# Performance work log

Hardware: AMD Instinct MI355X
Metric: run time of the kernel (lower is better)

The kernel has to match this reference:

```python
import jax, jax.numpy as jnp
import numpy as np

B, K, D, DS = 32, 64, 4, 4
H = 512            # hidden_dim
HH = H // 2        # hidden_hidden_dim = 256
NA = 2             # n_action


def _lin(k, out_d, in_d):
    kw, kb = jax.random.split(k)
    w = jax.random.normal(kw, (out_d, in_d), dtype=jnp.float32) * (in_d ** -0.5)
    b = jax.random.normal(kb, (out_d,), dtype=jnp.float32) * 0.01
    return w, b


def setup_inputs() -> dict:
    key = jax.random.key(0)
    ks = jax.random.split(key, 16)
    state = jax.random.normal(ks[0], (B, DS), dtype=jnp.float32)
    obs = jax.random.normal(ks[1], (B, D, K), dtype=jnp.float32)
    layer_w, layer_b = _lin(ks[2], H, DS)
    e1_w, e1_b = _lin(ks[3], H, 2 * D)
    e2_w, e2_b = _lin(ks[4], H, H)
    e3_w, e3_b = _lin(ks[5], H, H)
    ln_g = jnp.ones((H,), jnp.float32)
    ln_b = jnp.zeros((H,), jnp.float32)
    n1_w, n1_b = _lin(ks[6], H, D + H + DS)
    n2_w, n2_b = _lin(ks[7], HH, H)
    mu1_w, mu1_b = _lin(ks[8], 256, H + H)
    mu2_w, mu2_b = _lin(ks[9], 128, 256)
    mu3_w, mu3_b = _lin(ks[10], NA, 128)
    s1_w, s1_b = _lin(ks[11], 256, H + H)
    s2_w, s2_b = _lin(ks[12], 128, 256)
    s3_w, s3_b = _lin(ks[13], NA, 128)
    return dict(state=state, obs=obs, layer_w=layer_w, layer_b=layer_b,
                e1_w=e1_w, e1_b=e1_b, e2_w=e2_w, e2_b=e2_b, e3_w=e3_w, e3_b=e3_b,
                ln_g=ln_g, ln_b=ln_b, n1_w=n1_w, n1_b=n1_b, n2_w=n2_w, n2_b=n2_b,
                mu1_w=mu1_w, mu1_b=mu1_b, mu2_w=mu2_w, mu2_b=mu2_b, mu3_w=mu3_w, mu3_b=mu3_b,
                s1_w=s1_w, s1_b=s1_b, s2_w=s2_w, s2_b=s2_b, s3_w=s3_w, s3_b=s3_b)


def _dense(x, w, b):
    return x @ w.T + b


def reference(state, obs, layer_w, layer_b, e1_w, e1_b, e2_w, e2_b, e3_w, e3_b,
              ln_g, ln_b, n1_w, n1_b, n2_w, n2_b,
              mu1_w, mu1_b, mu2_w, mu2_b, mu3_w, mu3_b,
              s1_w, s1_b, s2_w, s2_b, s3_w, s3_b):
    # ---- InteractionNetwork ----
    o = jnp.transpose(obs, (0, 2, 1))                       # [B,K,D]
    mask = jnp.sum(jnp.abs(o), axis=2) != 0                 # [B,K] bool
    counts = jnp.clip(jnp.sum(mask, axis=1, keepdims=True).astype(o.dtype), 1e-6)  # [B,1]
    # all-pairs edge features [B,K,K,2D]
    obs_i = jnp.broadcast_to(o[:, :, None, :], (B, K, K, D))
    obs_j = jnp.broadcast_to(o[:, None, :, :], (B, K, K, D))
    edge_input = jnp.concatenate([obs_i, obs_j], axis=-1)
    h = jax.nn.relu(_dense(edge_input, e1_w, e1_b))
    h = jax.nn.relu(_dense(h, e2_w, e2_b))
    edge_output = jax.nn.relu(_dense(h, e3_w, e3_b))        # [B,K,K,H]
    edge_mask = (mask[:, :, None] & mask[:, None, :]).astype(o.dtype)  # [B,K,K]
    edge_output = edge_output * edge_mask[..., None]
    valid_counts = jnp.clip(jnp.sum(edge_mask, axis=2, keepdims=True), 1e-6)  # [B,K,1]
    agg = jnp.sum(edge_output, axis=2) / valid_counts       # [B,K,H]
    # LayerNorm (eps=1e-5, torch default)
    mu_ = jnp.mean(agg, axis=-1, keepdims=True)
    var_ = jnp.mean((agg - mu_) ** 2, axis=-1, keepdims=True)
    agg = (agg - mu_) * jax.lax.rsqrt(var_ + 1e-5) * ln_g + ln_b
    st_exp = jnp.broadcast_to(state[:, None, :], (B, K, DS))
    node_input = jnp.concatenate([o, agg, st_exp], axis=-1)  # [B,K,D+H+DS]
    node_output = _dense(jax.nn.relu(_dense(node_input, n1_w, n1_b)), n2_w, n2_b)  # [B,K,HH]
    m3 = mask[:, :, None]
    mean_pool = jnp.sum(jnp.where(m3, node_output, 0.0), axis=1) / counts  # [B,HH]
    max_pool = jnp.max(jnp.where(m3, node_output, -1e9), axis=1)           # [B,HH]
    obs_feat = jnp.concatenate([mean_pool, max_pool], axis=-1)             # [B,H]
    # ---- ActorNetwork head ----
    st_feat = jax.nn.relu(_dense(state, layer_w, layer_b))                 # [B,H]
    x = jnp.concatenate([st_feat, obs_feat], axis=1)                       # [B,2H]
    mu = _dense(jax.nn.relu(_dense(jax.nn.relu(_dense(x, mu1_w, mu1_b)), mu2_w, mu2_b)), mu3_w, mu3_b)
    std = jax.nn.softplus(_dense(jax.nn.relu(_dense(jax.nn.relu(_dense(x, s1_w, s1_b)), s2_w, s2_b)), s3_w, s3_b))
    std = jnp.clip(std + 0.001, 0.1, 2.0)
    return mu, std
```

## Files before the change

### kernel.cpp

```cpp
#include <hip/hip_runtime.h>
#include <hip/hip_fp16.h>

typedef _Float16 f16x8 __attribute__((ext_vector_type(8)));
typedef _Float16 f16x4 __attribute__((ext_vector_type(4)));
typedef float f32x4 __attribute__((ext_vector_type(4)));

#define NB 32
#define NK 64
#define ND 4
#define NH 512
#define NKP 544


__global__ void prep_obs_kernel(const float* __restrict__ obs,
                                const float* __restrict__ state,
                                float* __restrict__ o,
                                float* __restrict__ maskp,
                                float* __restrict__ cntp,
                                _Float16* __restrict__ nodein) {
  const int b = blockIdx.x;
  const int j = threadIdx.x;
  float o0 = obs[(b*4 + 0)*64 + j];
  float o1 = obs[(b*4 + 1)*64 + j];
  float o2 = obs[(b*4 + 2)*64 + j];
  float o3 = obs[(b*4 + 3)*64 + j];
  size_t bi = (size_t)b*64 + j;
  float* orow = o + bi*4;
  orow[0] = o0; orow[1] = o1; orow[2] = o2; orow[3] = o3;
  float s = fabsf(o0) + fabsf(o1) + fabsf(o2) + fabsf(o3);
  float m = (s != 0.0f) ? 1.0f : 0.0f;
  maskp[bi] = m;
  float c = m;
  #pragma unroll
  for (int off = 1; off < 64; off <<= 1) c += __shfl_xor(c, off);
  if (j == 0) cntp[b] = fmaxf(c, 1e-6f);
  _Float16* nrow = nodein + bi*NKP;
  nrow[0] = (_Float16)o0; nrow[1] = (_Float16)o1;
  nrow[2] = (_Float16)o2; nrow[3] = (_Float16)o3;
  nrow[516] = (_Float16)state[b*4 + 0];
  nrow[517] = (_Float16)state[b*4 + 1];
  nrow[518] = (_Float16)state[b*4 + 2];
  nrow[519] = (_Float16)state[b*4 + 3];
  for (int k2 = 520; k2 < 544; ++k2) nrow[k2] = (_Float16)0.0f;
}

__global__ void prep_uv16(const float* __restrict__ o,
                          const float* __restrict__ e1w,
                          const float* __restrict__ e1b,
                          _Float16* __restrict__ u16,
                          _Float16* __restrict__ v16) {
  const int bi = blockIdx.x;
  const int c = threadIdx.x;
  const float* orow = o + (size_t)bi*4;
  float o0 = orow[0], o1 = orow[1], o2 = orow[2], o3 = orow[3];
  const float* wr = e1w + c*8;
  float u = wr[0]*o0 + wr[1]*o1 + wr[2]*o2 + wr[3]*o3 + e1b[c];
  float v = wr[4]*o0 + wr[5]*o1 + wr[6]*o2 + wr[7]*o3;
  u16[(size_t)bi*NH + c] = (_Float16)u;
  v16[(size_t)bi*NH + c] = (_Float16)v;
}

__global__ void prep_w16_kernel(const float* __restrict__ e2w,
                                const float* __restrict__ e3w,
                                const float* __restrict__ n2w,
                                const float* __restrict__ n1w,
                                _Float16* __restrict__ w2h,
                                _Float16* __restrict__ w3h,
                                _Float16* __restrict__ n2wh,
                                _Float16* __restrict__ n1wh) {
  int idx = blockIdx.x * blockDim.x + threadIdx.x;
  const int A = 512*512, Bc = 512*512, C = 256*512, Dn = 512*544;
  if (idx < A) {
    w2h[idx] = (_Float16)e2w[idx];
  } else if (idx < A + Bc) {
    int q = idx - A; w3h[q] = (_Float16)e3w[q];
  } else if (idx < A + Bc + C) {
    int q = idx - A - Bc; n2wh[q] = (_Float16)n2w[q];
  } else if (idx < A + Bc + C + Dn) {
    int q = idx - A - Bc - C;
    int n = q / 544, k = q % 544;
    n1wh[q] = (k < 520) ? (_Float16)n1w[n*520 + k] : (_Float16)0.0f;
  }
}

__global__ void prep_stfeat_kernel(const float* __restrict__ state,
                                   const float* __restrict__ lw,
                                   const float* __restrict__ lb,
                                   float* __restrict__ xfeat) {
  const int b = blockIdx.x, c = threadIdx.x;
  const float* s = state + b*4;
  const float* wr = lw + c*4;
  float hv = wr[0]*s[0] + wr[1]*s[1] + wr[2]*s[2] + wr[3]*s[3] + lb[c];
  xfeat[b*1024 + c] = fmaxf(hv, 0.0f);
}


__device__ __forceinline__ void mlp_layer(const char* hb,
                                          const _Float16* __restrict__ wbase0,
                                          const float* __restrict__ biasp,
                                          int wcol, int lr, int lg,
                                          f32x4 acc[8][4]) {
  #pragma unroll
  for (int nt = 0; nt < 4; ++nt) {
    float bz = biasp[wcol + nt*16 + lr];
    #pragma unroll
    for (int mt = 0; mt < 8; ++mt) {
      acc[mt][nt][0] = bz; acc[mt][nt][1] = bz;
      acc[mt][nt][2] = bz; acc[mt][nt][3] = bz;
    }
  }
  const _Float16* bbase = wbase0 + (size_t)(wcol + lr)*NH + lg*8;
  f16x8 bfp[4];
  #pragma unroll
  for (int nt = 0; nt < 4; ++nt)
    bfp[nt] = *(const f16x8*)(bbase + nt*16*NH);
  for (int kk = 0; kk < 16; ++kk) {
    f16x8 bf[4];
    #pragma unroll
    for (int nt = 0; nt < 4; ++nt) bf[nt] = bfp[nt];
    if (kk < 15) {
      #pragma unroll
      for (int nt = 0; nt < 4; ++nt)
        bfp[nt] = *(const f16x8*)(bbase + nt*16*NH + (kk+1)*32);
    }
    f16x8 af[8];
    #pragma unroll
    for (int mt = 0; mt < 8; ++mt) {
      const int row = mt*16 + lr;
      af[mt] = *(const f16x8*)(hb + ((row*1024 + kk*64 + lg*16) ^ ((row & 7) << 4)));
    }
    #pragma unroll
    for (int mt = 0; mt < 8; ++mt)
      #pragma unroll
      for (int nt = 0; nt < 4; ++nt)
        acc[mt][nt] = __builtin_amdgcn_mfma_f32_16x16x32_f16(af[mt], bf[nt], acc[mt][nt], 0, 0, 0);
  }
}

__global__ __launch_bounds__(512, 1) void edge_fused(
    const _Float16* __restrict__ u16, const _Float16* __restrict__ v16,
    const _Float16* __restrict__ w2h, const _Float16* __restrict__ w3h,
    const float* __restrict__ e2b, const float* __restrict__ e3b,
    const float* __restrict__ maskp, const float* __restrict__ cntp,
    const float* __restrict__ lng, const float* __restrict__ lnb,
    _Float16* __restrict__ nodein) {
  __shared__ __align__(16) char lds[131072];
  __shared__ float em_s[64];
  __shared__ float red_s[16];
  __shared__ float stat_s[2];

  const int t = threadIdx.x;
  const int bi0 = blockIdx.x * 2;
  const int b = bi0 >> 6;
  const int w = t >> 6, l = t & 63, lr = l & 15, lg = l >> 4;
  const int wcol = w * 64;

  if (t < 64) em_s[t] = maskp[(size_t)b*64 + t];

  {
    const int jrow = t >> 3;
    const int kc = t & 7;
    const _Float16* vrow = v16 + ((size_t)(b*64 + jrow))*NH + kc*64;
    const _Float16* u0p  = u16 + (size_t)bi0*NH + kc*64;
    const _Float16* u1p  = u16 + (size_t)(bi0 + 1)*NH + kc*64;
    #pragma unroll
    for (int e8 = 0; e8 < 8; ++e8) {
      f16x8 vv = *(const f16x8*)(vrow + e8*8);
      f16x8 u0 = *(const f16x8*)(u0p + e8*8);
      f16x8 u1 = *(const f16x8*)(u1p + e8*8);
      f16x8 h0, h1;
      #pragma unroll
      for (int e = 0; e < 8; ++e) {
        _Float16 x0 = u0[e] + vv[e];
        _Float16 x1 = u1[e] + vv[e];
        h0[e] = x0 > (_Float16)0 ? x0 : (_Float16)0;
        h1[e] = x1 > (_Float16)0 ? x1 : (_Float16)0;
      }
      const int bc = (kc*64 + e8*8)*2;
      const int r1 = 64 + jrow;
      *(f16x8*)(lds + ((jrow*1024 + bc) ^ ((jrow & 7) << 4))) = h0;
      *(f16x8*)(lds + ((r1*1024 + bc) ^ ((r1 & 7) << 4))) = h1;
    }
  }
  __syncthreads();

  f32x4 acc[8][4];

  mlp_layer(lds, w2h, e2b, wcol, lr, lg, acc);
  __syncthreads();

  #pragma unroll
  for (int mt = 0; mt < 8; ++mt)
    #pragma unroll
    for (int nt = 0; nt < 4; ++nt)
      #pragma unroll
      for (int r = 0; r < 4; ++r) {
        int row = mt*16 + lg*4 + r;
        int cc = wcol + nt*16 + lr;
        *(_Float16*)(lds + ((row*1024 + cc*2) ^ ((row & 7) << 4))) =
            (_Float16)fmaxf(acc[mt][nt][r], 0.0f);
      }
  __syncthreads();

  mlp_layer(lds, w3h, e3b, wcol, lr, lg, acc);

  float csum[2][4] = {{0.f,0.f,0.f,0.f},{0.f,0.f,0.f,0.f}};
  #pragma unroll
  for (int mt = 0; mt < 8; ++mt) {
    const int g = mt >> 2;
    float em0 = em_s[(mt&3)*16 + lg*4 + 0];
    float em1 = em_s[(mt&3)*16 + lg*4 + 1];
    float em2 = em_s[(mt&3)*16 + lg*4 + 2];
    float em3 = em_s[(mt&3)*16 + lg*4 + 3];
    #pragma unroll
    for (int nt = 0; nt < 4; ++nt) {
      csum[g][nt] += em0 * fmaxf(acc[mt][nt][0], 0.f)
                   + em1 * fmaxf(acc[mt][nt][1], 0.f)
                   + em2 * fmaxf(acc[mt][nt][2], 0.f)
                   + em3 * fmaxf(acc[mt][nt][3], 0.f);
    }
  }
  #pragma unroll
  for (int g = 0; g < 2; ++g)
    #pragma unroll
    for (int nt = 0; nt < 4; ++nt) {
      csum[g][nt] += __shfl_xor(csum[g][nt], 16);
      csum[g][nt] += __shfl_xor(csum[g][nt], 32);
    }
  float cnt = cntp[b];
  __syncthreads();
  float* aggs = (float*)lds;
  if (lg == 0) {
    #pragma unroll
    for (int g = 0; g < 2; ++g) {
      int big = bi0 + g;
      float sc = em_s[big & 63] / cnt;
      #pragma unroll
      for (int nt = 0; nt < 4; ++nt)
        aggs[g*512 + wcol + nt*16 + lr] = csum[g][nt] * sc;
    }
  }
  __syncthreads();

  for (int g = 0; g < 2; ++g) {
    float a = aggs[g*512 + t];
    float s1 = a, s2 = a * a;
    #pragma unroll
    for (int off = 1; off < 64; off <<= 1) {
      s1 += __shfl_xor(s1, off);
      s2 += __shfl_xor(s2, off);
    }
    if (l == 0) { red_s[w] = s1; red_s[8 + w] = s2; }
    __syncthreads();
    if (t == 0) {
      float S1 = 0.f, S2 = 0.f;
      #pragma unroll
      for (int q = 0; q < 8; ++q) { S1 += red_s[q]; S2 += red_s[8 + q]; }
      float mean = S1 * (1.0f/512.0f);
      float var = S2 * (1.0f/512.0f) - mean * mean;
      stat_s[0] = mean;
      stat_s[1] = rsqrtf(var + 1e-5f);
    }
    __syncthreads();
    float nrm = (a - stat_s[0]) * stat_s[1] * lng[t] + lnb[t];
    nodein[(size_t)(bi0 + g)*NKP + 4 + t] = (_Float16)nrm;
    __syncthreads();
  }
}


template <int RELU16>
__global__ __launch_bounds__(256) void node_gemm(
    const _Float16* __restrict__ A, const _Float16* __restrict__ Bw,
    const float* __restrict__ bias, void* __restrict__ outp,
    int Ka, int ldo) {
  const int t = threadIdx.x;
  const int w = t >> 6, l = t & 63, lr = l & 15, lg = l >> 4;
  const int m0 = blockIdx.x * 64;
  const int col = blockIdx.y * 64 + w*16 + lr;
  f32x4 acc[4];
  float bz = bias[col];
  #pragma unroll
  for (int mt = 0; mt < 4; ++mt) {
    acc[mt][0] = bz; acc[mt][1] = bz; acc[mt][2] = bz; acc[mt][3] = bz;
  }
  const _Float16* bptr = Bw + (size_t)col*Ka + lg*8;
  const _Float16* aptr = A + (size_t)(m0 + lr)*Ka + lg*8;
  const int nkk = Ka >> 5;
  for (int kk = 0; kk < nkk; ++kk) {
    f16x8 bf = *(const f16x8*)(bptr + kk*32);
    #pragma unroll
    for (int mt = 0; mt < 4; ++mt) {
      f16x8 af = *(const f16x8*)(aptr + ((size_t)mt*16)*Ka + kk*32);
      acc[mt] = __builtin_amdgcn_mfma_f32_16x16x32_f16(af, bf, acc[mt], 0, 0, 0);
    }
  }
  #pragma unroll
  for (int mt = 0; mt < 4; ++mt)
    #pragma unroll
    for (int r = 0; r < 4; ++r) {
      int row = m0 + mt*16 + lg*4 + r;
      float vv = acc[mt][r];
      if (RELU16)
        ((_Float16*)outp)[(size_t)row*ldo + col] = (_Float16)fmaxf(vv, 0.f);
      else
        ((float*)outp)[(size_t)row*ldo + col] = vv;
    }
}


__global__ __launch_bounds__(256) void pool_kernel(
    const float* __restrict__ nodeout, const float* __restrict__ maskp,
    const float* __restrict__ cntp, float* __restrict__ xfeat) {
  const int b = blockIdx.x;
  const int c = threadIdx.x;
  float sum = 0.f, mx = -1e9f;
  for (int i = 0; i < 64; ++i) {
    float m = maskp[b*64 + i];
    float v = nodeout[((size_t)(b*64 + i))*256 + c];
    sum += m * v;
    mx = fmaxf(mx, (m != 0.f) ? v : -1e9f);
  }
  xfeat[b*1024 + 512 + c] = sum / cntp[b];
  xfeat[b*1024 + 768 + c] = mx;
}

__global__ __launch_bounds__(256) void heads_g1(
    const float* __restrict__ xfeat,
    const float* __restrict__ mu1w, const float* __restrict__ s1w,
    float* __restrict__ part) {
  __shared__ __align__(16) float xs[256];
  const int b = blockIdx.x, h = blockIdx.y, ks = blockIdx.z;
  const int t = threadIdx.x;
  xs[t] = xfeat[b*1024 + ks*256 + t];
  __syncthreads();
  const float* wr = (h ? s1w : mu1w) + (size_t)t*1024 + ks*256;
  float a = 0.f;
  #pragma unroll 8
  for (int k = 0; k < 256; k += 4) {
    float4 ww = *(const float4*)(wr + k);
    float4 xx = *(const float4*)(xs + k);
    a += ww.x*xx.x + ww.y*xx.y + ww.z*xx.z + ww.w*xx.w;
  }
  part[(((size_t)(b*2 + h))*256 + t)*4 + ks] = a;
}

__global__ __launch_bounds__(256) void heads_g23(
    const float* __restrict__ part,
    const float* __restrict__ mu1b, const float* __restrict__ s1b,
    const float* __restrict__ mu2w, const float* __restrict__ mu2b,
    const float* __restrict__ s2w, const float* __restrict__ s2b,
    const float* __restrict__ mu3w, const float* __restrict__ mu3b,
    const float* __restrict__ s3w, const float* __restrict__ s3b,
    float* __restrict__ outp) {
  __shared__ __align__(16) float h1s[256];
  __shared__ __align__(16) float h2s[128];
  const int b = blockIdx.x, h = blockIdx.y;
  const int t = threadIdx.x;
  {
    float4 pp = *(const float4*)(part + (((size_t)(b*2 + h))*256 + t)*4);
    float a = pp.x + pp.y + pp.z + pp.w + (h ? s1b : mu1b)[t];
    h1s[t] = fmaxf(a, 0.f);
  }
  __syncthreads();
  {
    const int o = t >> 1, half = t & 1;
    const float* wr = (h ? s2w : mu2w) + (size_t)o*256 + half*128;
    const float* hp = h1s + half*128;
    float a = 0.f;
    #pragma unroll 8
    for (int k = 0; k < 128; k += 4) {
      float4 ww = *(const float4*)(wr + k);
      float4 hh = *(const float4*)(hp + k);
      a += ww.x*hh.x + ww.y*hh.y + ww.z*hh.z + ww.w*hh.w;
    }
    a += __shfl_xor(a, 1);
    if (half == 0) h2s[o] = fmaxf(a + (h ? s2b : mu2b)[o], 0.f);
  }
  __syncthreads();
  if (t < 64) {
    const int o = t >> 5, lane = t & 31;
    const float* wr = (h ? s3w : mu3w) + o*128 + lane*4;
    const float* hp = h2s + lane*4;
    float4 ww = *(const float4*)wr;
    float4 hh = *(const float4*)hp;
    float a = ww.x*hh.x + ww.y*hh.y + ww.z*hh.z + ww.w*hh.w;
    #pragma unroll
    for (int off = 1; off < 32; off <<= 1) a += __shfl_xor(a, off);
    if (lane == 0) {
      a += (h ? s3b : mu3b)[o];
      if (h == 0) {
        outp[b*2 + o] = a;
      } else {
        float spv = (a > 0.f) ? (a + log1pf(expf(-a))) : log1pf(expf(a));
        outp[64 + b*2 + o] = fminf(fmaxf(spv + 0.001f, 0.1f), 2.0f);
      }
    }
  }
}


extern "C" void kernel_launch(void* const* d_in, const int* in_sizes, int n_in,
                              void* d_out, int out_size, void* d_ws, size_t ws_size,
                              hipStream_t stream) {
  const float* state  = (const float*)d_in[0];
  const float* obs    = (const float*)d_in[1];
  const float* layerw = (const float*)d_in[2];
  const float* layerb = (const float*)d_in[3];
  const float* e1w    = (const float*)d_in[4];
  const float* e1b    = (const float*)d_in[5];
  const float* e2w    = (const float*)d_in[6];
  const float* e2b    = (const float*)d_in[7];
  const float* e3w    = (const float*)d_in[8];
  const float* e3b    = (const float*)d_in[9];
  const float* lng    = (const float*)d_in[10];
  const float* lnb    = (const float*)d_in[11];
  const float* n1w    = (const float*)d_in[12];
  const float* n1b    = (const float*)d_in[13];
  const float* n2w    = (const float*)d_in[14];
  const float* n2b    = (const float*)d_in[15];
  const float* mu1w   = (const float*)d_in[16];
  const float* mu1b   = (const float*)d_in[17];
  const float* mu2w   = (const float*)d_in[18];
  const float* mu2b   = (const float*)d_in[19];
  const float* mu3w   = (const float*)d_in[20];
  const float* mu3b   = (const float*)d_in[21];
  const float* s1w    = (const float*)d_in[22];
  const float* s1b    = (const float*)d_in[23];
  const float* s2w    = (const float*)d_in[24];
  const float* s2b    = (const float*)d_in[25];
  const float* s3w    = (const float*)d_in[26];
  const float* s3b    = (const float*)d_in[27];
  float* outp = (float*)d_out;

  char* p = (char*)d_ws;
  auto alloc = [&](size_t bytes) {
    char* r = p;
    p += (bytes + 255) & ~(size_t)255;
    return r;
  };
  float*    o       = (float*)alloc((size_t)2048*4*4);
  float*    maskp   = (float*)alloc((size_t)2048*4);
  float*    cntp    = (float*)alloc((size_t)32*4);
  _Float16* u16     = (_Float16*)alloc((size_t)2048*512*2);
  _Float16* v16     = (_Float16*)alloc((size_t)2048*512*2);
  _Float16* w2h     = (_Float16*)alloc((size_t)512*512*2);
  _Float16* w3h     = (_Float16*)alloc((size_t)512*512*2);
  _Float16* nodein  = (_Float16*)alloc((size_t)2048*544*2);
  _Float16* n1wh    = (_Float16*)alloc((size_t)512*544*2);
  _Float16* n2wh    = (_Float16*)alloc((size_t)256*512*2);
  _Float16* nodeh   = (_Float16*)alloc((size_t)2048*512*2);
  float*    nodeout = (float*)alloc((size_t)2048*256*4);
  float*    xfeat   = (float*)alloc((size_t)32*1024*4);
  float*    hpart   = (float*)alloc((size_t)32*2*256*4*4);

  prep_obs_kernel<<<32, 64, 0, stream>>>(obs, state, o, maskp, cntp, nodein);
  prep_uv16<<<2048, 512, 0, stream>>>(o, e1w, e1b, u16, v16);
  prep_w16_kernel<<<3648, 256, 0, stream>>>(e2w, e3w, n2w, n1w, w2h, w3h, n2wh, n1wh);
  prep_stfeat_kernel<<<32, 512, 0, stream>>>(state, layerw, layerb, xfeat);

  edge_fused<<<1024, 512, 0, stream>>>(u16, v16, w2h, w3h, e2b, e3b,
                                       maskp, cntp, lng, lnb, nodein);

  node_gemm<1><<<dim3(32, 8), 256, 0, stream>>>(nodein, n1wh, n1b, (void*)nodeh, 544, 512);
  node_gemm<0><<<dim3(32, 4), 256, 0, stream>>>(nodeh, n2wh, n2b, (void*)nodeout, 512, 256);
  pool_kernel<<<32, 256, 0, stream>>>(nodeout, maskp, cntp, xfeat);
  heads_g1<<<dim3(32, 2, 4), 256, 0, stream>>>(xfeat, mu1w, s1w, hpart);
  heads_g23<<<dim3(32, 2), 256, 0, stream>>>(hpart, mu1b, s1b, mu2w, mu2b,
                                             s2w, s2b, mu3w, mu3b, s3w, s3b, outp);
}
```

Measured before the change: 240.1 us.

## Software-pipeline A-fragment LDS loads, coalesce edge-input loads, batch uv prep

The MFMA inner loop now splits the eight row tiles into two halves. It prefetches the next k-step's low-half A fragments while the high half computes, and raises wave priority around the MFMA bursts with s_setprio. The edge-input staging loop now uses interleaved slots so adjacent threads read contiguous global memory. prep_uv16 launches one block per batch and loops over 64 rows, so each thread loads its weights once instead of using 2048 tiny blocks. Together these aim to hide LDS latency, improve coalescing and cut launch/block overhead, at the cost of more registers in an already register-heavy kernel and less parallelism in the prep kernel.

```diff
diff --git a/kernel.cpp b/kernel.cpp
--- a/kernel.cpp
+++ b/kernel.cpp
@@ -44,20 +44,27 @@
   for (int k2 = 520; k2 < 544; ++k2) nrow[k2] = (_Float16)0.0f;
 }
 
-__global__ void prep_uv16(const float* __restrict__ o,
-                          const float* __restrict__ e1w,
-                          const float* __restrict__ e1b,
-                          _Float16* __restrict__ u16,
-                          _Float16* __restrict__ v16) {
-  const int bi = blockIdx.x;
+__global__ __launch_bounds__(512) void prep_uv16(
+    const float* __restrict__ o,
+    const float* __restrict__ e1w,
+    const float* __restrict__ e1b,
+    _Float16* __restrict__ u16,
+    _Float16* __restrict__ v16) {
+  const int b = blockIdx.x;
   const int c = threadIdx.x;
-  const float* orow = o + (size_t)bi*4;
-  float o0 = orow[0], o1 = orow[1], o2 = orow[2], o3 = orow[3];
   const float* wr = e1w + c*8;
-  float u = wr[0]*o0 + wr[1]*o1 + wr[2]*o2 + wr[3]*o3 + e1b[c];
-  float v = wr[4]*o0 + wr[5]*o1 + wr[6]*o2 + wr[7]*o3;
-  u16[(size_t)bi*NH + c] = (_Float16)u;
-  v16[(size_t)bi*NH + c] = (_Float16)v;
+  float4 wa = *(const float4*)wr;
+  float4 wb = *(const float4*)(wr + 4);
+  float bias = e1b[c];
+  for (int j = 0; j < 64; ++j) {
+    const int bi = b*64 + j;
+    const float* orow = o + (size_t)bi*4;
+    float4 ov = *(const float4*)orow;
+    float u = wa.x*ov.x + wa.y*ov.y + wa.z*ov.z + wa.w*ov.w + bias;
+    float v = wb.x*ov.x + wb.y*ov.y + wb.z*ov.z + wb.w*ov.w;
+    u16[(size_t)bi*NH + c] = (_Float16)u;
+    v16[(size_t)bi*NH + c] = (_Float16)v;
+  }
 }
 
 __global__ void prep_w16_kernel(const float* __restrict__ e2w,
@@ -114,6 +121,14 @@
   #pragma unroll
   for (int nt = 0; nt < 4; ++nt)
     bfp[nt] = *(const f16x8*)(bbase + nt*16*NH);
+
+  f16x8 aflo[4];
+  #pragma unroll
+  for (int mt = 0; mt < 4; ++mt) {
+    const int row = mt*16 + lr;
+    aflo[mt] = *(const f16x8*)(hb + ((row*1024 + lg*16) ^ ((row & 7) << 4)));
+  }
+
   for (int kk = 0; kk < 16; ++kk) {
     f16x8 bf[4];
     #pragma unroll
@@ -123,17 +138,36 @@
       for (int nt = 0; nt < 4; ++nt)
         bfp[nt] = *(const f16x8*)(bbase + nt*16*NH + (kk+1)*32);
     }
-    f16x8 af[8];
-    #pragma unroll
-    for (int mt = 0; mt < 8; ++mt) {
-      const int row = mt*16 + lr;
-      af[mt] = *(const f16x8*)(hb + ((row*1024 + kk*64 + lg*16) ^ ((row & 7) << 4)));
-    }
-    #pragma unroll
-    for (int mt = 0; mt < 8; ++mt)
+    f16x8 afhi[4];
+    #pragma unroll
+    for (int mt = 0; mt < 4; ++mt) {
+      const int row = (mt + 4)*16 + lr;
+      afhi[mt] = *(const f16x8*)(hb + ((row*1024 + kk*64 + lg*16) ^ ((row & 7) << 4)));
+    }
+    __builtin_amdgcn_s_setprio(1);
+    #pragma unroll
+    for (int mt = 0; mt < 4; ++mt)
       #pragma unroll
       for (int nt = 0; nt < 4; ++nt)
-        acc[mt][nt] = __builtin_amdgcn_mfma_f32_16x16x32_f16(af[mt], bf[nt], acc[mt][nt], 0, 0, 0);
+        acc[mt][nt] = __builtin_amdgcn_mfma_f32_16x16x32_f16(aflo[mt], bf[nt], acc[mt][nt], 0, 0, 0);
+    __builtin_amdgcn_s_setprio(0);
+    f16x8 aflon[4];
+    if (kk < 15) {
+      #pragma unroll
+      for (int mt = 0; mt < 4; ++mt) {
+        const int row = mt*16 + lr;
+        aflon[mt] = *(const f16x8*)(hb + ((row*1024 + (kk+1)*64 + lg*16) ^ ((row & 7) << 4)));
+      }
+    }
+    __builtin_amdgcn_s_setprio(1);
+    #pragma unroll
+    for (int mt = 0; mt < 4; ++mt)
+      #pragma unroll
+      for (int nt = 0; nt < 4; ++nt)
+        acc[mt + 4][nt] = __builtin_amdgcn_mfma_f32_16x16x32_f16(afhi[mt], bf[nt], acc[mt + 4][nt], 0, 0, 0);
+    __builtin_amdgcn_s_setprio(0);
+    #pragma unroll
+    for (int mt = 0; mt < 4; ++mt) aflo[mt] = aflon[mt];
   }
 }
 
@@ -159,24 +193,25 @@
 
   {
     const int jrow = t >> 3;
-    const int kc = t & 7;
-    const _Float16* vrow = v16 + ((size_t)(b*64 + jrow))*NH + kc*64;
-    const _Float16* u0p  = u16 + (size_t)bi0*NH + kc*64;
-    const _Float16* u1p  = u16 + (size_t)(bi0 + 1)*NH + kc*64;
-    #pragma unroll
-    for (int e8 = 0; e8 < 8; ++e8) {
-      f16x8 vv = *(const f16x8*)(vrow + e8*8);
-      f16x8 u0 = *(const f16x8*)(u0p + e8*8);
-      f16x8 u1 = *(const f16x8*)(u1p + e8*8);
+    const int slot = t & 7;
+    const _Float16* vrow = v16 + ((size_t)(b*64 + jrow))*NH;
+    const _Float16* u0p  = u16 + (size_t)bi0*NH;
+    const _Float16* u1p  = u16 + (size_t)(bi0 + 1)*NH;
+    #pragma unroll
+    for (int e = 0; e < 8; ++e) {
+      const int kelem = e*64 + slot*8;
+      f16x8 vv = *(const f16x8*)(vrow + kelem);
+      f16x8 u0 = *(const f16x8*)(u0p + kelem);
+      f16x8 u1 = *(const f16x8*)(u1p + kelem);
       f16x8 h0, h1;
       #pragma unroll
-      for (int e = 0; e < 8; ++e) {
-        _Float16 x0 = u0[e] + vv[e];
-        _Float16 x1 = u1[e] + vv[e];
-        h0[e] = x0 > (_Float16)0 ? x0 : (_Float16)0;
-        h1[e] = x1 > (_Float16)0 ? x1 : (_Float16)0;
+      for (int q = 0; q < 8; ++q) {
+        _Float16 x0 = u0[q] + vv[q];
+        _Float16 x1 = u1[q] + vv[q];
+        h0[q] = x0 > (_Float16)0 ? x0 : (_Float16)0;
+        h1[q] = x1 > (_Float16)0 ? x1 : (_Float16)0;
       }
-      const int bc = (kc*64 + e8*8)*2;
+      const int bc = kelem*2;
       const int r1 = 64 + jrow;
       *(f16x8*)(lds + ((jrow*1024 + bc) ^ ((jrow & 7) << 4))) = h0;
       *(f16x8*)(lds + ((r1*1024 + bc) ^ ((r1 & 7) << 4))) = h1;
@@ -455,7 +490,7 @@
   float*    hpart   = (float*)alloc((size_t)32*2*256*4*4);
 
   prep_obs_kernel<<<32, 64, 0, stream>>>(obs, state, o, maskp, cntp, nodein);
-  prep_uv16<<<2048, 512, 0, stream>>>(o, e1w, e1b, u16, v16);
+  prep_uv16<<<32, 512, 0, stream>>>(o, e1w, e1b, u16, v16);
   prep_w16_kernel<<<3648, 256, 0, stream>>>(e2w, e3w, n2w, n1w, w2h, w3h, n2wh, n1wh);
   prep_stfeat_kernel<<<32, 512, 0, stream>>>(state, layerw, layerb, xfeat);
 
```

New measurement: 230.1 us. -4.2%, faster.
